# Kernel optimization log

Hardware: AMD Instinct MI355X
Metric: run time of the kernel (lower is better)

Reference implementation:

```python
import jax, jax.numpy as jnp
import numpy as np
import math

D = 1024
H = 16
HD = D // H
P = 64  # bias_proj_dim
B, N, M = 4, 1024, 2048
EPS_LN = 1e-5
EPS_NORM = 1e-12


def _ln(x, g, b):
    mu = jnp.mean(x, axis=-1, keepdims=True)
    var = jnp.var(x, axis=-1, keepdims=True)
    return (x - mu) * jax.lax.rsqrt(var + EPS_LN) * g + b


def _l2norm_dim1(x):
    # torch F.normalize(x, p=2) default dim=1 -> normalize over the sequence axis
    n = jnp.sqrt(jnp.sum(x * x, axis=1, keepdims=True))
    return x / jnp.maximum(n, EPS_NORM)


def setup_inputs() -> dict:
    key = jax.random.key(0)
    ks = jax.random.split(key, 16)
    s = 1.0 / math.sqrt(D)
    inp = {
        'dataset_features': jax.random.normal(ks[0], (B, N, D), jnp.float32),
        'visual_features': jax.random.normal(ks[1], (B, M, D), jnp.float32),
        # linear weights stored as (in, out): y = x @ W + b
        'wq_w': jax.random.normal(ks[2], (D, D), jnp.float32) * s,
        'wq_b': jnp.zeros((D,), jnp.float32),
        'wk_w': jax.random.normal(ks[3], (D, D), jnp.float32) * s,
        'wk_b': jnp.zeros((D,), jnp.float32),
        'wv_w': jax.random.normal(ks[4], (D, D), jnp.float32) * s,
        'wv_b': jnp.zeros((D,), jnp.float32),
        'wo_w': jax.random.normal(ks[5], (D, D), jnp.float32) * s,
        'wo_b': jnp.zeros((D,), jnp.float32),
        'gq_w': jax.random.normal(ks[6], (D, P), jnp.float32) * s,
        'gq_b': jnp.zeros((P,), jnp.float32),
        'gk_w': jax.random.normal(ks[7], (D, P), jnp.float32) * s,
        'gk_b': jnp.zeros((P,), jnp.float32),
        'pos_scale': jnp.asarray(2.0, jnp.float32),
        'neg_scale': jnp.asarray(50.0, jnp.float32),
        'attn_logit_scale': jnp.asarray(math.log(10.0), jnp.float32),
        'ln_q_g': jnp.ones((D,), jnp.float32),
        'ln_q_b': jnp.zeros((D,), jnp.float32),
        'ln_kv_g': jnp.ones((D,), jnp.float32),
        'ln_kv_b': jnp.zeros((D,), jnp.float32),
        'ln_out_g': jnp.ones((D,), jnp.float32),
        'ln_out_b': jnp.zeros((D,), jnp.float32),
        'ff1_w': jax.random.normal(ks[8], (D, 2 * D), jnp.float32) * s,
        'ff1_b': jnp.zeros((2 * D,), jnp.float32),
        'ff2_w': jax.random.normal(ks[9], (2 * D, D), jnp.float32) * (1.0 / math.sqrt(2 * D)),
        'ff2_b': jnp.zeros((D,), jnp.float32),
    }
    return inp


def reference(dataset_features, visual_features, wq_w, wq_b, wk_w, wk_b, wv_w, wv_b,
              wo_w, wo_b, gq_w, gq_b, gk_w, gk_b, pos_scale, neg_scale,
              attn_logit_scale, ln_q_g, ln_q_b, ln_kv_g, ln_kv_b, ln_out_g, ln_out_b,
              ff1_w, ff1_b, ff2_w, ff2_b):
    residual = dataset_features
    q_in = _ln(dataset_features, ln_q_g, ln_q_b)   # [B,N,D]
    kv_in = _ln(visual_features, ln_kv_g, ln_kv_b)  # [B,M,D]

    geo_q = _l2norm_dim1(q_in @ gq_w + gq_b)   # [B,N,P], normalized over N
    geo_k = _l2norm_dim1(kv_in @ gk_w + gk_b)  # [B,M,P], normalized over M
    bias_raw = jnp.einsum('bnp,bmp->bnm', geo_q, geo_k)  # [B,N,M]
    full_bias = jax.nn.relu(bias_raw) * pos_scale - jax.nn.relu(-bias_raw) * neg_scale

    q = (q_in @ wq_w + wq_b).reshape(B, N, H, HD).transpose(0, 2, 1, 3)   # [B,H,N,hd]
    k = (kv_in @ wk_w + wk_b).reshape(B, M, H, HD).transpose(0, 2, 1, 3)  # [B,H,M,hd]
    v = (kv_in @ wv_w + wv_b).reshape(B, M, H, HD).transpose(0, 2, 1, 3)

    logits = jnp.einsum('bhnd,bhmd->bhnm', q, k) / math.sqrt(HD)
    logits = logits * jnp.exp(attn_logit_scale)
    scores = logits + full_bias[:, None, :, :]
    attn = jax.nn.softmax(scores, axis=-1)
    out = jnp.einsum('bhnm,bhmd->bhnd', attn, v).transpose(0, 2, 1, 3).reshape(B, N, D)
    out = out @ wo_w + wo_b
    out = residual + out

    residual = out
    h = _ln(out, ln_out_g, ln_out_b)
    ff = jax.nn.gelu(h @ ff1_w + ff1_b, approximate=False) @ ff2_w + ff2_b
    return residual + ff
```

## Files before the change

### kernel.cpp

```cpp
#include <hip/hip_runtime.h>


typedef __bf16 bf16x8 __attribute__((ext_vector_type(8)));
typedef __bf16 bf16x4 __attribute__((ext_vector_type(4)));
typedef float  f32x4  __attribute__((ext_vector_type(4)));

__device__ inline f32x4 mfma16(bf16x8 a, bf16x8 b, f32x4 c) {
  return __builtin_amdgcn_mfma_f32_16x16x32_bf16(a, b, c, 0, 0, 0);
}

__device__ inline void glds16(const void* g, void* l) {
  __builtin_amdgcn_global_load_lds(
      (const __attribute__((address_space(1))) void*)g,
      (__attribute__((address_space(3))) void*)l, 16, 0, 0);
}

__device__ inline int swz(int row, int col) {
  return row * 64 + ((((col >> 3) ^ (row & 7)) << 3) | (col & 7));
}

#define DB 1024
#define DH 16
#define DHD 64
#define DP 64
#define NB 4
#define NN 1024
#define NM 2048

__global__ __launch_bounds__(256) void k_transpose_all(
    const float* __restrict__ w0, const float* __restrict__ w1,
    const float* __restrict__ w2, const float* __restrict__ w3,
    const float* __restrict__ f1, const float* __restrict__ f2,
    const float* __restrict__ g0, const float* __restrict__ g1,
    __bf16* __restrict__ o0, __bf16* __restrict__ o1,
    __bf16* __restrict__ o2, __bf16* __restrict__ o3,
    __bf16* __restrict__ of1, __bf16* __restrict__ of2,
    __bf16* __restrict__ og0, __bf16* __restrict__ og1) {
  __shared__ float tile[32][33];
  int id = blockIdx.x;
  const float* in;
  __bf16* out;
  int K, O, x, y;
  if (id < 4096) {
    int mi = id >> 10, r = id & 1023;
    in = mi == 0 ? w0 : mi == 1 ? w1 : mi == 2 ? w2 : w3;
    out = mi == 0 ? o0 : mi == 1 ? o1 : mi == 2 ? o2 : o3;
    K = 1024; O = 1024; x = r & 31; y = r >> 5;
  } else if (id < 6144) {
    int r = id - 4096; in = f1; out = of1; K = 1024; O = 2048; x = r & 63; y = r >> 6;
  } else if (id < 8192) {
    int r = id - 6144; in = f2; out = of2; K = 2048; O = 1024; x = r & 31; y = r >> 5;
  } else if (id < 8256) {
    int r = id - 8192; in = g0; out = og0; K = 1024; O = 64; x = r & 1; y = r >> 1;
  } else {
    int r = id - 8256; in = g1; out = og1; K = 1024; O = 64; x = r & 1; y = r >> 1;
  }
  int k0 = y * 32, o0c = x * 32;
  int tx = threadIdx.x & 31, ty = threadIdx.x >> 5;
#pragma unroll
  for (int r = ty; r < 32; r += 8)
    tile[r][tx] = in[(size_t)(k0 + r) * O + (o0c + tx)];
  __syncthreads();
#pragma unroll
  for (int r = ty; r < 32; r += 8)
    out[(size_t)(o0c + r) * K + (k0 + tx)] = (__bf16)tile[tx][r];
}

__device__ inline void ln_body(const float* __restrict__ x,
                               const float* __restrict__ g,
                               const float* __restrict__ bb,
                               __bf16* __restrict__ y, size_t row) {
  int t = threadIdx.x;
  float4 v = ((const float4*)(x + row * 1024))[t];
  float s = v.x + v.y + v.z + v.w;
  float ss = v.x * v.x + v.y * v.y + v.z * v.z + v.w * v.w;
#pragma unroll
  for (int o = 32; o; o >>= 1) {
    s += __shfl_down(s, o, 64);
    ss += __shfl_down(ss, o, 64);
  }
  __shared__ float r1[4], r2[4];
  if ((t & 63) == 0) { r1[t >> 6] = s; r2[t >> 6] = ss; }
  __syncthreads();
  s = r1[0] + r1[1] + r1[2] + r1[3];
  ss = r2[0] + r2[1] + r2[2] + r2[3];
  float mu = s * (1.f / 1024.f);
  float rstd = rsqrtf(ss * (1.f / 1024.f) - mu * mu + 1e-5f);
  float4 gv = ((const float4*)g)[t];
  float4 bv = ((const float4*)bb)[t];
  __bf16* yr = y + row * 1024 + t * 4;
  yr[0] = (__bf16)((v.x - mu) * rstd * gv.x + bv.x);
  yr[1] = (__bf16)((v.y - mu) * rstd * gv.y + bv.y);
  yr[2] = (__bf16)((v.z - mu) * rstd * gv.z + bv.z);
  yr[3] = (__bf16)((v.w - mu) * rstd * gv.w + bv.w);
}

__global__ __launch_bounds__(256) void k_layernorm(
    const float* __restrict__ x, const float* __restrict__ g,
    const float* __restrict__ bb, __bf16* __restrict__ y) {
  ln_body(x, g, bb, y, blockIdx.x);
}

__global__ __launch_bounds__(256) void k_layernorm2(
    const float* __restrict__ x1, const float* __restrict__ g1,
    const float* __restrict__ b1, __bf16* __restrict__ y1,
    const float* __restrict__ x2, const float* __restrict__ g2,
    const float* __restrict__ b2, __bf16* __restrict__ y2) {
  int row = blockIdx.x;
  if (row < 4096) ln_body(x1, g1, b1, y1, row);
  else ln_body(x2, g2, b2, y2, row - 4096);
}

__global__ __launch_bounds__(256) void k_geo(
    const __bf16* __restrict__ qin, const __bf16* __restrict__ kvin,
    const __bf16* __restrict__ gqw, const __bf16* __restrict__ gkw,
    const float* __restrict__ gqb, const float* __restrict__ gkb,
    __bf16* __restrict__ geoq, __bf16* __restrict__ geok) {
  const int blk = blockIdx.x;
  const bool isq = blk < 128;
  const __bf16* A = isq ? qin : kvin;
  const __bf16* Bt = isq ? gqw : gkw;
  const float* bias = isq ? gqb : gkb;
  __bf16* C = isq ? geoq : geok;
  const int row0 = (isq ? blk : blk - 128) * 32;
  __shared__ __align__(16) __bf16 As[32][72], Bs[64][72];
  const int t = threadIdx.x, lane = t & 63, w = t >> 6;
  const int quad = lane >> 4, l15 = lane & 15;
  const int wr = w >> 1, wc = w & 1;
  const int sr = t >> 3, skc = (t & 7) * 8;
  const __bf16* aP = A + (size_t)(row0 + sr) * 1024 + skc;
  const __bf16* bP0 = Bt + (size_t)sr * 1024 + skc;
  const __bf16* bP1 = Bt + (size_t)(sr + 32) * 1024 + skc;
  bf16x8 av = *(const bf16x8*)aP;
  bf16x8 bv0 = *(const bf16x8*)bP0;
  bf16x8 bv1 = *(const bf16x8*)bP1;
  f32x4 acc[2] = {};
  for (int k0 = 0; k0 < 1024; k0 += 64) {
    __syncthreads();
    *(bf16x8*)&As[sr][skc] = av;
    *(bf16x8*)&Bs[sr][skc] = bv0;
    *(bf16x8*)&Bs[sr + 32][skc] = bv1;
    __syncthreads();
    if (k0 + 64 < 1024) {
      av = *(const bf16x8*)(aP + k0 + 64);
      bv0 = *(const bf16x8*)(bP0 + k0 + 64);
      bv1 = *(const bf16x8*)(bP1 + k0 + 64);
    }
#pragma unroll
    for (int ks = 0; ks < 2; ks++) {
      bf16x8 af = *(const bf16x8*)&As[wr * 16 + l15][ks * 32 + quad * 8];
#pragma unroll
      for (int ct = 0; ct < 2; ct++) {
        bf16x8 bfr = *(const bf16x8*)&Bs[wc * 32 + ct * 16 + l15][ks * 32 + quad * 8];
        acc[ct] = mfma16(af, bfr, acc[ct]);
      }
    }
  }
#pragma unroll
  for (int ct = 0; ct < 2; ct++) {
    int col = wc * 32 + ct * 16 + l15;
    float bc = bias[col];
#pragma unroll
    for (int i = 0; i < 4; i++) {
      int row = row0 + wr * 16 + quad * 4 + i;
      C[(size_t)row * 64 + col] = (__bf16)(acc[ct][i] + bc);
    }
  }
}

__global__ __launch_bounds__(256) void k_l2sum(
    const __bf16* __restrict__ gq, const __bf16* __restrict__ gk,
    float* __restrict__ sums) {
  int chunk = blockIdx.x, b = blockIdx.y, z = blockIdx.z;
  if (z == 0 && chunk >= 8) return;
  const __bf16* src = z ? gk : gq;
  int rows = z ? 2048 : 1024;
  const unsigned* base = (const unsigned*)(src + (size_t)b * rows * 64) + chunk * 128 * 32;
  int t = threadIdx.x, c = t & 31, ro = t >> 5;
  float s0 = 0.f, s1 = 0.f;
  for (int r = ro; r < 128; r += 8) {
    unsigned u = base[r * 32 + c];
    float f0 = __uint_as_float(u << 16);
    float f1 = __uint_as_float(u & 0xffff0000u);
    s0 += f0 * f0;
    s1 += f1 * f1;
  }
  __shared__ float ls[64];
  if (t < 64) ls[t] = 0.f;
  __syncthreads();
  atomicAdd(&ls[c * 2], s0);
  atomicAdd(&ls[c * 2 + 1], s1);
  __syncthreads();
  if (t < 64) atomicAdd(&sums[z * 256 + b * 64 + t], ls[t]);
}

__global__ __launch_bounds__(256) void k_l2scale(
    __bf16* __restrict__ gk, const float* __restrict__ sums) {
  int chunk = blockIdx.x, b = blockIdx.y;
  unsigned* base = (unsigned*)(gk + (size_t)b * 2048 * 64) + chunk * 128 * 32;
  int t = threadIdx.x, c = t & 31, ro = t >> 5;
  float sq0 = sums[b * 64 + c * 2], sq1 = sums[b * 64 + c * 2 + 1];
  float sk0 = sums[256 + b * 64 + c * 2], sk1 = sums[256 + b * 64 + c * 2 + 1];
  float m0 = 1.f / (fmaxf(sqrtf(sq0), 1e-12f) * fmaxf(sqrtf(sk0), 1e-12f));
  float m1 = 1.f / (fmaxf(sqrtf(sq1), 1e-12f) * fmaxf(sqrtf(sk1), 1e-12f));
  for (int r = ro; r < 128; r += 8) {
    unsigned u = base[r * 32 + c];
    float f0 = __uint_as_float(u << 16) * m0;
    float f1 = __uint_as_float(u & 0xffff0000u) * m1;
    unsigned short h0 = __builtin_bit_cast(unsigned short, (__bf16)f0);
    unsigned short h1 = __builtin_bit_cast(unsigned short, (__bf16)f1);
    base[r * 32 + c] = (unsigned)h0 | ((unsigned)h1 << 16);
  }
}

__global__ __launch_bounds__(256, 3) void k_qkv(
    const __bf16* __restrict__ qin, const __bf16* __restrict__ kvin,
    const __bf16* __restrict__ twq, const __bf16* __restrict__ twk,
    const __bf16* __restrict__ twv, const float* __restrict__ qbias,
    const float* __restrict__ kbias, const float* __restrict__ vbias,
    __bf16* __restrict__ qb, __bf16* __restrict__ kb, __bf16* __restrict__ vtb) {
  int id = blockIdx.x;
  const __bf16 *A, *Bt;
  const float* bias;
  __bf16* C;
  int my, nx, Ndim;
  bool rowbias;
  if (id < 256) {
    A = qin; Bt = twq; bias = qbias; C = qb;
    nx = id & 7; my = id >> 3; Ndim = 1024; rowbias = false;
  } else if (id < 768) {
    id -= 256;
    A = kvin; Bt = twk; bias = kbias; C = kb;
    nx = id & 7; my = id >> 3; Ndim = 1024; rowbias = false;
  } else {
    id -= 768;
    A = twv; Bt = kvin; bias = vbias; C = vtb;
    nx = id & 63; my = id >> 6; Ndim = 8192; rowbias = true;
  }
  const int Kdim = 1024;
  __shared__ __align__(16) __bf16 As[128 * 32];
  __shared__ __align__(16) __bf16 Bs[128 * 32];
  const int m0 = my * 128, n0 = nx * 128;
  const int t = threadIdx.x, lane = t & 63, w = t >> 6;
  const int quad = lane >> 4, l15 = lane & 15;
  const int wr = w >> 1, wc = w & 1;
  const int srow = lane >> 2, scol = (lane & 3) * 8;
  const __bf16* aS0 = A + (size_t)(m0 + w * 32 + srow) * Kdim + scol;
  const __bf16* bS0 = Bt + (size_t)(n0 + w * 32 + srow) * Kdim + scol;
  const size_t K16 = (size_t)16 * Kdim;
  __bf16* lA0 = &As[(w * 32) * 32];
  __bf16* lB0 = &Bs[(w * 32) * 32];

  f32x4 acc[4][4] = {};
  for (int k0 = 0; k0 < Kdim; k0 += 32) {
    __syncthreads();
    glds16(aS0 + k0, lA0);
    glds16(aS0 + K16 + k0, lA0 + 16 * 32);
    glds16(bS0 + k0, lB0);
    glds16(bS0 + K16 + k0, lB0 + 16 * 32);
    __syncthreads();
    bf16x8 af[4], bg[4];
#pragma unroll
    for (int rt = 0; rt < 4; rt++)
      af[rt] = *(const bf16x8*)&As[(wr * 64 + rt * 16 + l15) * 32 + quad * 8];
#pragma unroll
    for (int ct = 0; ct < 4; ct++)
      bg[ct] = *(const bf16x8*)&Bs[(wc * 64 + ct * 16 + l15) * 32 + quad * 8];
#pragma unroll
    for (int rt = 0; rt < 4; rt++)
#pragma unroll
      for (int ct = 0; ct < 4; ct++)
        acc[rt][ct] = mfma16(af[rt], bg[ct], acc[rt][ct]);
  }
#pragma unroll
  for (int rt = 0; rt < 4; rt++) {
    int row = m0 + wr * 64 + rt * 16 + quad * 4;
#pragma unroll
    for (int ct = 0; ct < 4; ct++) {
      int col = n0 + wc * 64 + ct * 16 + l15;
      float bcol = rowbias ? 0.f : bias[col];
#pragma unroll
      for (int i = 0; i < 4; i++) {
        float vv = acc[rt][ct][i] + (rowbias ? bias[row + i] : bcol);
        C[(size_t)(row + i) * Ndim + col] = (__bf16)vv;
      }
    }
  }
}

__global__ __launch_bounds__(256, 3) void k_gemm128g(
    const __bf16* __restrict__ A, const __bf16* __restrict__ Bt,
    const float* __restrict__ bias, __bf16* __restrict__ Cout,
    int Ndim, int Kdim) {
  __shared__ __align__(16) __bf16 As[128 * 32];
  __shared__ __align__(16) __bf16 Bs[128 * 32];
  const int m0 = blockIdx.y * 128, n0 = blockIdx.x * 128;
  const int t = threadIdx.x, lane = t & 63, w = t >> 6;
  const int quad = lane >> 4, l15 = lane & 15;
  const int wr = w >> 1, wc = w & 1;
  const int srow = lane >> 2, scol = (lane & 3) * 8;
  const __bf16* aS0 = A + (size_t)(m0 + w * 32 + srow) * Kdim + scol;
  const __bf16* bS0 = Bt + (size_t)(n0 + w * 32 + srow) * Kdim + scol;
  const size_t K16 = (size_t)16 * Kdim;
  __bf16* lA0 = &As[(w * 32) * 32];
  __bf16* lB0 = &Bs[(w * 32) * 32];

  f32x4 acc[4][4] = {};
  for (int k0 = 0; k0 < Kdim; k0 += 32) {
    __syncthreads();
    glds16(aS0 + k0, lA0);
    glds16(aS0 + K16 + k0, lA0 + 16 * 32);
    glds16(bS0 + k0, lB0);
    glds16(bS0 + K16 + k0, lB0 + 16 * 32);
    __syncthreads();
    bf16x8 af[4], bg[4];
#pragma unroll
    for (int rt = 0; rt < 4; rt++)
      af[rt] = *(const bf16x8*)&As[(wr * 64 + rt * 16 + l15) * 32 + quad * 8];
#pragma unroll
    for (int ct = 0; ct < 4; ct++)
      bg[ct] = *(const bf16x8*)&Bs[(wc * 64 + ct * 16 + l15) * 32 + quad * 8];
#pragma unroll
    for (int rt = 0; rt < 4; rt++)
#pragma unroll
      for (int ct = 0; ct < 4; ct++)
        acc[rt][ct] = mfma16(af[rt], bg[ct], acc[rt][ct]);
  }
#pragma unroll
  for (int rt = 0; rt < 4; rt++) {
    int row = m0 + wr * 64 + rt * 16 + quad * 4;
#pragma unroll
    for (int ct = 0; ct < 4; ct++) {
      int col = n0 + wc * 64 + ct * 16 + l15;
      float bcol = bias[col];
#pragma unroll
      for (int i = 0; i < 4; i++) {
        float vv = acc[rt][ct][i] + bcol;
        Cout[(size_t)(row + i) * Ndim + col] =
            (__bf16)(0.5f * vv * (1.f + erff(vv * 0.70710678118f)));
      }
    }
  }
}

__global__ __launch_bounds__(256, 2) void k_gemmn64(
    const __bf16* __restrict__ A, const __bf16* __restrict__ Bt,
    const float* __restrict__ bias, const float* __restrict__ resid,
    float* __restrict__ Cout, int Ndim, int Kdim) {
  __shared__ __align__(16) __bf16 As[128 * 32];
  __shared__ __align__(16) __bf16 Bs[64 * 32];
  const int m0 = blockIdx.y * 128, n0 = blockIdx.x * 64;
  const int t = threadIdx.x, lane = t & 63, w = t >> 6;
  const int quad = lane >> 4, l15 = lane & 15;
  const int wr = w >> 1, wc = w & 1;
  const int srow = lane >> 2, scol = (lane & 3) * 8;
  const __bf16* aS0 = A + (size_t)(m0 + w * 32 + srow) * Kdim + scol;
  const __bf16* bS0 = Bt + (size_t)(n0 + w * 16 + srow) * Kdim + scol;
  const size_t K16 = (size_t)16 * Kdim;
  __bf16* lA0 = &As[(w * 32) * 32];
  __bf16* lB0 = &Bs[(w * 16) * 32];

  f32x4 acc[4][2] = {};
  for (int k0 = 0; k0 < Kdim; k0 += 32) {
    __syncthreads();
    glds16(aS0 + k0, lA0);
    glds16(aS0 + K16 + k0, lA0 + 16 * 32);
    glds16(bS0 + k0, lB0);
    __syncthreads();
    bf16x8 af[4], bg[2];
#pragma unroll
    for (int rt = 0; rt < 4; rt++)
      af[rt] = *(const bf16x8*)&As[(wr * 64 + rt * 16 + l15) * 32 + quad * 8];
#pragma unroll
    for (int ct = 0; ct < 2; ct++)
      bg[ct] = *(const bf16x8*)&Bs[(wc * 32 + ct * 16 + l15) * 32 + quad * 8];
#pragma unroll
    for (int rt = 0; rt < 4; rt++)
#pragma unroll
      for (int ct = 0; ct < 2; ct++)
        acc[rt][ct] = mfma16(af[rt], bg[ct], acc[rt][ct]);
  }
#pragma unroll
  for (int rt = 0; rt < 4; rt++) {
    int row = m0 + wr * 64 + rt * 16 + quad * 4;
#pragma unroll
    for (int ct = 0; ct < 2; ct++) {
      int col = n0 + wc * 32 + ct * 16 + l15;
      float bcol = bias[col];
#pragma unroll
      for (int i = 0; i < 4; i++) {
        size_t idx = (size_t)(row + i) * Ndim + col;
        Cout[idx] = acc[rt][ct][i] + bcol + resid[idx];
      }
    }
  }
}

__global__ __launch_bounds__(256, 2) void k_flash(
    const __bf16* __restrict__ Q, const __bf16* __restrict__ K,
    const __bf16* __restrict__ Vt, const __bf16* __restrict__ Gq,
    const __bf16* __restrict__ Gk, const float* __restrict__ als,
    const float* __restrict__ psc, const float* __restrict__ nsc,
    __bf16* __restrict__ Out) {
  const int o = blockIdx.x;
  const int bh = o & 63, x = o >> 6;
  const int b = bh & 3, h = bh >> 2;
  const int t = threadIdx.x, w = t >> 6, lane = t & 63;
  const int quad = lane >> 4, l15 = lane & 15;
  const int row0 = x * 128 + w * 32;
  const float LOG2E = 1.44269504089f;
  const float sc2 = __expf(als[0]) * 0.125f * LOG2E;
  const float pos2 = psc[0] * LOG2E, neg2 = nsc[0] * LOG2E;

  __shared__ __align__(16) __bf16 Ks[64 * 64];
  __shared__ __align__(16) __bf16 Gs[64 * 64];
  __shared__ __align__(16) __bf16 Vs[64 * 64];
  __shared__ __align__(16) __bf16 Ps[4][32 * 64];

  const __bf16* Qb = Q + ((size_t)(b * NN + row0)) * DB + h * DHD;
  const __bf16* Kb = K + ((size_t)b * NM) * DB + h * DHD;
  const __bf16* Vb = Vt + (size_t)(h * DHD) * (NB * NM) + (size_t)b * NM;
  const __bf16* Gqb = Gq + (size_t)(b * NN + row0) * DP;
  const __bf16* Gkb = Gk + (size_t)b * NM * DP;

  const int r0 = t >> 3, gc = (t & 7) * 8;
  const int sw0 = swz(r0, gc), sw1 = sw0 + 32 * 64;
  const int r1 = r0 + 32;

  bf16x8 qf[2][2], gqf[2][2];
#pragma unroll
  for (int rt = 0; rt < 2; rt++)
#pragma unroll
    for (int ks = 0; ks < 2; ks++) {
      qf[rt][ks] = *(const bf16x8*)(Qb + (size_t)(rt * 16 + l15) * DB + ks * 32 + quad * 8);
      gqf[rt][ks] = *(const bf16x8*)(Gqb + (size_t)(rt * 16 + l15) * DP + ks * 32 + quad * 8);
    }

  bf16x8 kst0 = *(const bf16x8*)(Kb + (size_t)r0 * DB + gc);
  bf16x8 kst1 = *(const bf16x8*)(Kb + (size_t)r1 * DB + gc);
  bf16x8 gst0 = *(const bf16x8*)(Gkb + (size_t)r0 * DP + gc);
  bf16x8 gst1 = *(const bf16x8*)(Gkb + (size_t)r1 * DP + gc);
  bf16x8 vst0 = *(const bf16x8*)(Vb + (size_t)r0 * (NB * NM) + gc);
  bf16x8 vst1 = *(const bf16x8*)(Vb + (size_t)r1 * (NB * NM) + gc);

  float lrowq[2] = {};
  f32x4 oacc[2][4] = {};
  f32x4 z4 = {0.f, 0.f, 0.f, 0.f};

  for (int m0 = 0; m0 < NM; m0 += 64) {
    __syncthreads();
    *(bf16x8*)&Ks[sw0] = kst0;
    *(bf16x8*)&Ks[sw1] = kst1;
    *(bf16x8*)&Gs[sw0] = gst0;
    *(bf16x8*)&Gs[sw1] = gst1;
    *(bf16x8*)&Vs[sw0] = vst0;
    *(bf16x8*)&Vs[sw1] = vst1;
    __syncthreads();
    if (m0 + 64 < NM) {
      kst0 = *(const bf16x8*)(Kb + (size_t)(m0 + 64 + r0) * DB + gc);
      kst1 = *(const bf16x8*)(Kb + (size_t)(m0 + 64 + r1) * DB + gc);
      gst0 = *(const bf16x8*)(Gkb + (size_t)(m0 + 64 + r0) * DP + gc);
      gst1 = *(const bf16x8*)(Gkb + (size_t)(m0 + 64 + r1) * DP + gc);
      vst0 = *(const bf16x8*)(Vb + (size_t)r0 * (NB * NM) + m0 + 64 + gc);
      vst1 = *(const bf16x8*)(Vb + (size_t)r1 * (NB * NM) + m0 + 64 + gc);
    }
    bf16x8 kf[4][2], gkf[4][2];
#pragma unroll
    for (int ct = 0; ct < 4; ct++)
#pragma unroll
      for (int ks = 0; ks < 2; ks++) {
        int off = swz(ct * 16 + l15, ks * 32 + quad * 8);
        kf[ct][ks] = *(const bf16x8*)&Ks[off];
        gkf[ct][ks] = *(const bf16x8*)&Gs[off];
      }
#pragma unroll
    for (int ct = 0; ct < 4; ct++)
#pragma unroll
      for (int rt = 0; rt < 2; rt++) {
        f32x4 s = mfma16(kf[ct][1], qf[rt][1], mfma16(kf[ct][0], qf[rt][0], z4));
        f32x4 bg = mfma16(gkf[ct][1], gqf[rt][1], mfma16(gkf[ct][0], gqf[rt][0], z4));
        bf16x4 pk;
        float part = 0.f;
#pragma unroll
        for (int i = 0; i < 4; i++) {
          float bb = bg[i];
          float scl = bb > 0.f ? pos2 : neg2;
          float p = __builtin_amdgcn_exp2f(fmaf(bb, scl, s[i] * sc2));
          part += p;
          pk[i] = (__bf16)p;
        }
        lrowq[rt] += part;
        *(bf16x4*)&Ps[w][swz(rt * 16 + l15, ct * 16 + quad * 4)] = pk;
      }
    bf16x8 pf[2][2], vf[4][2];
#pragma unroll
    for (int rt = 0; rt < 2; rt++)
#pragma unroll
      for (int ms = 0; ms < 2; ms++)
        pf[rt][ms] = *(const bf16x8*)&Ps[w][swz(rt * 16 + l15, ms * 32 + quad * 8)];
#pragma unroll
    for (int dt = 0; dt < 4; dt++)
#pragma unroll
      for (int ms = 0; ms < 2; ms++)
        vf[dt][ms] = *(const bf16x8*)&Vs[swz(dt * 16 + l15, ms * 32 + quad * 8)];
#pragma unroll
    for (int rt = 0; rt < 2; rt++)
#pragma unroll
      for (int dt = 0; dt < 4; dt++) {
        oacc[rt][dt] = mfma16(pf[rt][0], vf[dt][0], oacc[rt][dt]);
        oacc[rt][dt] = mfma16(pf[rt][1], vf[dt][1], oacc[rt][dt]);
      }
  }
  float ltot[2];
#pragma unroll
  for (int rt = 0; rt < 2; rt++) {
    float l = lrowq[rt];
    l += __shfl_xor(l, 16, 64);
    l += __shfl_xor(l, 32, 64);
    ltot[rt] = l;
  }
#pragma unroll
  for (int rt = 0; rt < 2; rt++)
#pragma unroll
    for (int i = 0; i < 4; i++) {
      float li = __shfl(ltot[rt], quad * 4 + i, 64);
      float inv = 1.f / li;
#pragma unroll
      for (int dt = 0; dt < 4; dt++)
        Out[(size_t)(b * NN + row0 + rt * 16 + quad * 4 + i) * DB + h * DHD + dt * 16 + l15] =
            (__bf16)(oacc[rt][dt][i] * inv);
    }
}

extern "C" void kernel_launch(void* const* d_in, const int* in_sizes, int n_in,
                              void* d_out, int out_size, void* d_ws, size_t ws_size,
                              hipStream_t stream) {
  const float* dataset = (const float*)d_in[0];
  const float* visual = (const float*)d_in[1];
  const float* wq_w = (const float*)d_in[2];
  const float* wq_b = (const float*)d_in[3];
  const float* wk_w = (const float*)d_in[4];
  const float* wk_b = (const float*)d_in[5];
  const float* wv_w = (const float*)d_in[6];
  const float* wv_b = (const float*)d_in[7];
  const float* wo_w = (const float*)d_in[8];
  const float* wo_b = (const float*)d_in[9];
  const float* gq_w = (const float*)d_in[10];
  const float* gq_b = (const float*)d_in[11];
  const float* gk_w = (const float*)d_in[12];
  const float* gk_b = (const float*)d_in[13];
  const float* pos_scale = (const float*)d_in[14];
  const float* neg_scale = (const float*)d_in[15];
  const float* als = (const float*)d_in[16];
  const float* ln_q_g = (const float*)d_in[17];
  const float* ln_q_b = (const float*)d_in[18];
  const float* ln_kv_g = (const float*)d_in[19];
  const float* ln_kv_b = (const float*)d_in[20];
  const float* ln_out_g = (const float*)d_in[21];
  const float* ln_out_b = (const float*)d_in[22];
  const float* ff1_w = (const float*)d_in[23];
  const float* ff1_b = (const float*)d_in[24];
  const float* ff2_w = (const float*)d_in[25];
  const float* ff2_b = (const float*)d_in[26];

  char* ws = (char*)d_ws;
  size_t off = 0;
  auto alloc = [&](size_t bytes) {
    size_t o = off;
    off += (bytes + 255) & ~(size_t)255;
    return o;
  };
  __bf16* t_wq = (__bf16*)(ws + alloc((size_t)1024 * 1024 * 2));
  __bf16* t_wk = (__bf16*)(ws + alloc((size_t)1024 * 1024 * 2));
  __bf16* t_wv = (__bf16*)(ws + alloc((size_t)1024 * 1024 * 2));
  __bf16* t_wo = (__bf16*)(ws + alloc((size_t)1024 * 1024 * 2));
  __bf16* t_ff1 = (__bf16*)(ws + alloc((size_t)2048 * 1024 * 2));
  __bf16* t_ff2 = (__bf16*)(ws + alloc((size_t)1024 * 2048 * 2));
  __bf16* t_gq = (__bf16*)(ws + alloc((size_t)64 * 1024 * 2));
  __bf16* t_gk = (__bf16*)(ws + alloc((size_t)64 * 1024 * 2));
  size_t qin_off = alloc((size_t)4096 * 1024 * 2);
  size_t kvin_off = alloc((size_t)8192 * 1024 * 2);
  __bf16* qin = (__bf16*)(ws + qin_off);
  __bf16* kvin = (__bf16*)(ws + kvin_off);
  __bf16* geoq = (__bf16*)(ws + alloc((size_t)4096 * 64 * 2));
  __bf16* geok = (__bf16*)(ws + alloc((size_t)8192 * 64 * 2));
  float* sums = (float*)(ws + alloc((size_t)2 * 4 * 64 * 4));
  __bf16* qb = (__bf16*)(ws + alloc((size_t)4096 * 1024 * 2));
  __bf16* kb = (__bf16*)(ws + alloc((size_t)8192 * 1024 * 2));
  __bf16* vtb = (__bf16*)(ws + alloc((size_t)1024 * 8192 * 2));
  __bf16* attn = (__bf16*)(ws + alloc((size_t)4096 * 1024 * 2));
  __bf16* ffh = (__bf16*)(ws + alloc((size_t)4096 * 2048 * 2));
  float* out1 = (float*)(ws + kvin_off);
  __bf16* hbuf = (__bf16*)(ws + qin_off);
  float* outp = (float*)d_out;

  dim3 blk(256);
  k_transpose_all<<<8320, blk, 0, stream>>>(wq_w, wk_w, wv_w, wo_w, ff1_w, ff2_w,
                                            gq_w, gk_w, t_wq, t_wk, t_wv, t_wo,
                                            t_ff1, t_ff2, t_gq, t_gk);
  k_layernorm2<<<12288, blk, 0, stream>>>(dataset, ln_q_g, ln_q_b, qin,
                                          visual, ln_kv_g, ln_kv_b, kvin);
  k_geo<<<384, blk, 0, stream>>>(qin, kvin, t_gq, t_gk, gq_b, gk_b, geoq, geok);
  hipMemsetAsync(sums, 0, 2 * 4 * 64 * 4, stream);
  k_l2sum<<<dim3(16, 4, 2), blk, 0, stream>>>(geoq, geok, sums);
  k_l2scale<<<dim3(16, 4), blk, 0, stream>>>(geok, sums);
  k_qkv<<<1280, blk, 0, stream>>>(qin, kvin, t_wq, t_wk, t_wv,
                                  wq_b, wk_b, wv_b, qb, kb, vtb);
  k_flash<<<512, blk, 0, stream>>>(qb, kb, vtb, geoq, geok, als,
                                   pos_scale, neg_scale, attn);
  k_gemmn64<<<dim3(16, 32), blk, 0, stream>>>(attn, t_wo, wo_b, dataset, out1,
                                              1024, 1024);
  k_layernorm<<<4096, blk, 0, stream>>>(out1, ln_out_g, ln_out_b, hbuf);
  k_gemm128g<<<dim3(16, 32), blk, 0, stream>>>(hbuf, t_ff1, ff1_b, ffh,
                                               2048, 1024);
  k_gemmn64<<<dim3(16, 32), blk, 0, stream>>>(ffh, t_ff2, ff2_b, out1, outp,
                                              1024, 2048);
}
```

Measured before the change: 439.6 us.

## Precompute geometric bias matrix once instead of per-head in flash kernel

Adds a kernel that computes the relu-scaled geometric bias for each batch once and writes it as a bf16 [B,N,M] buffer. The flash kernel then reads the bias tiles from global memory instead of recomputing the geo dot products for every head. This removes 16x redundant bias MFMAs and the Gs LDS staging. In exchange it adds a 16 MB intermediate that is written once and read 16 times, with uncoalesced 8-byte loads inside the flash loop. Rounding the bias to bf16 slightly changes precision.

```diff
diff --git a/kernel.cpp b/kernel.cpp
--- a/kernel.cpp
+++ b/kernel.cpp
@@ -213,6 +213,44 @@
   }
 }
 
+__global__ __launch_bounds__(256) void k_bias(
+    const __bf16* __restrict__ gq, const __bf16* __restrict__ gk,
+    const float* __restrict__ psc, const float* __restrict__ nsc,
+    __bf16* __restrict__ Bias) {
+  const int mt0 = blockIdx.x * 128, nt0 = blockIdx.y * 128, b = blockIdx.z;
+  const int t = threadIdx.x, lane = t & 63, w = t >> 6;
+  const int quad = lane >> 4, l15 = lane & 15;
+  const int wm = w & 1, wn = w >> 1;
+  const float LOG2E = 1.44269504089f;
+  const float pos2 = psc[0] * LOG2E, neg2 = nsc[0] * LOG2E;
+  const __bf16* gqb = gq + (size_t)(b * NN + nt0 + wn * 64) * DP;
+  const __bf16* gkb = gk + (size_t)(b * NM + mt0 + wm * 64) * DP;
+  bf16x8 af[4][2], bg[4][2];
+#pragma unroll
+  for (int i = 0; i < 4; i++)
+#pragma unroll
+    for (int ks = 0; ks < 2; ks++) {
+      af[i][ks] = *(const bf16x8*)(gkb + (size_t)(i * 16 + l15) * DP + ks * 32 + quad * 8);
+      bg[i][ks] = *(const bf16x8*)(gqb + (size_t)(i * 16 + l15) * DP + ks * 32 + quad * 8);
+    }
+  __bf16* ob = Bias + (size_t)(b * NN + nt0 + wn * 64) * NM + mt0 + wm * 64;
+#pragma unroll
+  for (int nt = 0; nt < 4; nt++)
+#pragma unroll
+    for (int mt = 0; mt < 4; mt++) {
+      f32x4 acc = {};
+      acc = mfma16(af[mt][0], bg[nt][0], acc);
+      acc = mfma16(af[mt][1], bg[nt][1], acc);
+      bf16x4 o;
+#pragma unroll
+      for (int i = 0; i < 4; i++) {
+        float x = acc[i];
+        o[i] = (__bf16)(x > 0.f ? x * pos2 : x * neg2);
+      }
+      *(bf16x4*)(ob + (size_t)(nt * 16 + l15) * NM + mt * 16 + quad * 4) = o;
+    }
+}
+
 __global__ __launch_bounds__(256, 3) void k_qkv(
     const __bf16* __restrict__ qin, const __bf16* __restrict__ kvin,
     const __bf16* __restrict__ twq, const __bf16* __restrict__ twk,
@@ -398,10 +436,8 @@
 
 __global__ __launch_bounds__(256, 2) void k_flash(
     const __bf16* __restrict__ Q, const __bf16* __restrict__ K,
-    const __bf16* __restrict__ Vt, const __bf16* __restrict__ Gq,
-    const __bf16* __restrict__ Gk, const float* __restrict__ als,
-    const float* __restrict__ psc, const float* __restrict__ nsc,
-    __bf16* __restrict__ Out) {
+    const __bf16* __restrict__ Vt, const __bf16* __restrict__ Bias,
+    const float* __restrict__ als, __bf16* __restrict__ Out) {
   const int o = blockIdx.x;
   const int bh = o & 63, x = o >> 6;
   const int b = bh & 3, h = bh >> 2;
@@ -410,36 +446,29 @@
   const int row0 = x * 128 + w * 32;
   const float LOG2E = 1.44269504089f;
   const float sc2 = __expf(als[0]) * 0.125f * LOG2E;
-  const float pos2 = psc[0] * LOG2E, neg2 = nsc[0] * LOG2E;
 
   __shared__ __align__(16) __bf16 Ks[64 * 64];
-  __shared__ __align__(16) __bf16 Gs[64 * 64];
   __shared__ __align__(16) __bf16 Vs[64 * 64];
   __shared__ __align__(16) __bf16 Ps[4][32 * 64];
 
   const __bf16* Qb = Q + ((size_t)(b * NN + row0)) * DB + h * DHD;
   const __bf16* Kb = K + ((size_t)b * NM) * DB + h * DHD;
   const __bf16* Vb = Vt + (size_t)(h * DHD) * (NB * NM) + (size_t)b * NM;
-  const __bf16* Gqb = Gq + (size_t)(b * NN + row0) * DP;
-  const __bf16* Gkb = Gk + (size_t)b * NM * DP;
+  const __bf16* Bb = Bias + (size_t)(b * NN + row0) * NM;
 
   const int r0 = t >> 3, gc = (t & 7) * 8;
   const int sw0 = swz(r0, gc), sw1 = sw0 + 32 * 64;
   const int r1 = r0 + 32;
 
-  bf16x8 qf[2][2], gqf[2][2];
+  bf16x8 qf[2][2];
 #pragma unroll
   for (int rt = 0; rt < 2; rt++)
 #pragma unroll
-    for (int ks = 0; ks < 2; ks++) {
+    for (int ks = 0; ks < 2; ks++)
       qf[rt][ks] = *(const bf16x8*)(Qb + (size_t)(rt * 16 + l15) * DB + ks * 32 + quad * 8);
-      gqf[rt][ks] = *(const bf16x8*)(Gqb + (size_t)(rt * 16 + l15) * DP + ks * 32 + quad * 8);
-    }
 
   bf16x8 kst0 = *(const bf16x8*)(Kb + (size_t)r0 * DB + gc);
   bf16x8 kst1 = *(const bf16x8*)(Kb + (size_t)r1 * DB + gc);
-  bf16x8 gst0 = *(const bf16x8*)(Gkb + (size_t)r0 * DP + gc);
-  bf16x8 gst1 = *(const bf16x8*)(Gkb + (size_t)r1 * DP + gc);
   bf16x8 vst0 = *(const bf16x8*)(Vb + (size_t)r0 * (NB * NM) + gc);
   bf16x8 vst1 = *(const bf16x8*)(Vb + (size_t)r1 * (NB * NM) + gc);
 
@@ -451,41 +480,38 @@
     __syncthreads();
     *(bf16x8*)&Ks[sw0] = kst0;
     *(bf16x8*)&Ks[sw1] = kst1;
-    *(bf16x8*)&Gs[sw0] = gst0;
-    *(bf16x8*)&Gs[sw1] = gst1;
     *(bf16x8*)&Vs[sw0] = vst0;
     *(bf16x8*)&Vs[sw1] = vst1;
     __syncthreads();
+    bf16x4 btv[4][2];
+#pragma unroll
+    for (int ct = 0; ct < 4; ct++)
+#pragma unroll
+      for (int rt = 0; rt < 2; rt++)
+        btv[ct][rt] = *(const bf16x4*)(Bb + (size_t)(rt * 16 + l15) * NM +
+                                       m0 + ct * 16 + quad * 4);
     if (m0 + 64 < NM) {
       kst0 = *(const bf16x8*)(Kb + (size_t)(m0 + 64 + r0) * DB + gc);
       kst1 = *(const bf16x8*)(Kb + (size_t)(m0 + 64 + r1) * DB + gc);
-      gst0 = *(const bf16x8*)(Gkb + (size_t)(m0 + 64 + r0) * DP + gc);
-      gst1 = *(const bf16x8*)(Gkb + (size_t)(m0 + 64 + r1) * DP + gc);
       vst0 = *(const bf16x8*)(Vb + (size_t)r0 * (NB * NM) + m0 + 64 + gc);
       vst1 = *(const bf16x8*)(Vb + (size_t)r1 * (NB * NM) + m0 + 64 + gc);
     }
-    bf16x8 kf[4][2], gkf[4][2];
+    bf16x8 kf[4][2];
 #pragma unroll
     for (int ct = 0; ct < 4; ct++)
 #pragma unroll
-      for (int ks = 0; ks < 2; ks++) {
-        int off = swz(ct * 16 + l15, ks * 32 + quad * 8);
-        kf[ct][ks] = *(const bf16x8*)&Ks[off];
-        gkf[ct][ks] = *(const bf16x8*)&Gs[off];
-      }
+      for (int ks = 0; ks < 2; ks++)
+        kf[ct][ks] = *(const bf16x8*)&Ks[swz(ct * 16 + l15, ks * 32 + quad * 8)];
 #pragma unroll
     for (int ct = 0; ct < 4; ct++)
 #pragma unroll
       for (int rt = 0; rt < 2; rt++) {
         f32x4 s = mfma16(kf[ct][1], qf[rt][1], mfma16(kf[ct][0], qf[rt][0], z4));
-        f32x4 bg = mfma16(gkf[ct][1], gqf[rt][1], mfma16(gkf[ct][0], gqf[rt][0], z4));
         bf16x4 pk;
         float part = 0.f;
 #pragma unroll
         for (int i = 0; i < 4; i++) {
-          float bb = bg[i];
-          float scl = bb > 0.f ? pos2 : neg2;
-          float p = __builtin_amdgcn_exp2f(fmaf(bb, scl, s[i] * sc2));
+          float p = __builtin_amdgcn_exp2f(fmaf(s[i], sc2, (float)btv[ct][rt][i]));
           part += p;
           pk[i] = (__bf16)p;
         }
@@ -585,6 +611,7 @@
   __bf16* geoq = (__bf16*)(ws + alloc((size_t)4096 * 64 * 2));
   __bf16* geok = (__bf16*)(ws + alloc((size_t)8192 * 64 * 2));
   float* sums = (float*)(ws + alloc((size_t)2 * 4 * 64 * 4));
+  __bf16* biasb = (__bf16*)(ws + alloc((size_t)4096 * 2048 * 2));
   __bf16* qb = (__bf16*)(ws + alloc((size_t)4096 * 1024 * 2));
   __bf16* kb = (__bf16*)(ws + alloc((size_t)8192 * 1024 * 2));
   __bf16* vtb = (__bf16*)(ws + alloc((size_t)1024 * 8192 * 2));
@@ -604,10 +631,11 @@
   hipMemsetAsync(sums, 0, 2 * 4 * 64 * 4, stream);
   k_l2sum<<<dim3(16, 4, 2), blk, 0, stream>>>(geoq, geok, sums);
   k_l2scale<<<dim3(16, 4), blk, 0, stream>>>(geok, sums);
+  k_bias<<<dim3(16, 8, 4), blk, 0, stream>>>(geoq, geok, pos_scale, neg_scale,
+                                             biasb);
   k_qkv<<<1280, blk, 0, stream>>>(qin, kvin, t_wq, t_wk, t_wv,
                                   wq_b, wk_b, wv_b, qb, kb, vtb);
-  k_flash<<<512, blk, 0, stream>>>(qb, kb, vtb, geoq, geok, als,
-                                   pos_scale, neg_scale, attn);
+  k_flash<<<512, blk, 0, stream>>>(qb, kb, vtb, biasb, als, attn);
   k_gemmn64<<<dim3(16, 32), blk, 0, stream>>>(attn, t_wo, wo_b, dataset, out1,
                                               1024, 1024);
   k_layernorm<<<4096, blk, 0, stream>>>(out1, ln_out_g, ln_out_b, hbuf);
```

Measured after the change: 451.7 us. 1.03x slower.
